# Kernel tuning notes

Hardware: AMD Instinct MI355X
Metric: run time of the kernel (lower is better)

Reference implementation:

```python
import jax, jax.numpy as jnp
import numpy as np

B, T, C = 32, 1024, 256   # T must equal block_size for the mask broadcast to be valid
HS = 64                   # head_size


def setup_inputs() -> dict:
    key = jax.random.key(0)
    kx, kk, kq, kv = jax.random.split(key, 4)
    s = 1.0 / np.sqrt(C)  # nn.Linear default-ish scale
    return {
        "x": jax.random.normal(kx, (B, T, C), dtype=jnp.float32),
        "Wk": jax.random.uniform(kk, (HS, C), dtype=jnp.float32, minval=-s, maxval=s),
        "Wq": jax.random.uniform(kq, (HS, C), dtype=jnp.float32, minval=-s, maxval=s),
        "Wv": jax.random.uniform(kv, (HS, C), dtype=jnp.float32, minval=-s, maxval=s),
    }


def reference(x, Wk, Wq, Wv):
    # projections: nn.Linear(bias=False) -> x @ W^T
    k = jnp.einsum('btc,hc->bth', x, Wk)  # [B,T,HS]
    q = jnp.einsum('btc,hc->bth', x, Wq)
    v = jnp.einsum('btc,hc->bth', x, Wv)
    # fresh cache + T == block_size  =>  k_cache = k, v_cache = v
    wei = jnp.einsum('bth,bsh->bts', q, k) / np.sqrt(HS)  # [B,T,T]
    causal = jnp.tril(jnp.ones((T, T), dtype=bool))
    wei = jnp.where(causal, wei, -jnp.inf)
    wei = jax.nn.softmax(wei, axis=-1)  # dropout p=0 -> identity
    out = jnp.einsum('bts,bsh->bth', wei, v)  # [B,T,HS]
    return out
```

## Files before the change

### kernel.cpp

```cpp
#include <hip/hip_runtime.h>
#include <hip/hip_bf16.h>
#include <math.h>


#define B_  32
#define T_  1024
#define C_  256
#define HS_ 64
#define QSCALE 0.1803368801111204f

typedef __attribute__((ext_vector_type(8))) short bf16x8;
typedef __attribute__((ext_vector_type(4))) float f32x4;

static __device__ __forceinline__ unsigned short f2bf(float f) {
    unsigned u = __builtin_bit_cast(unsigned, f);
    u += 0x7FFFu + ((u >> 16) & 1u);
    return (unsigned short)(u >> 16);
}
static __device__ __forceinline__ unsigned pack_bf2(float a, float b) {
    unsigned ua = __builtin_bit_cast(unsigned, a) + 0x8000u;
    unsigned ub = __builtin_bit_cast(unsigned, b) + 0x8000u;
    return __builtin_amdgcn_perm(ub, ua, 0x07060302u);
}
static __device__ __forceinline__ bf16x8 cvt8r(float4 v0, float4 v1) {
    union { bf16x8 v; unsigned u[4]; } t;
    t.u[0] = pack_bf2(v0.x, v0.y); t.u[1] = pack_bf2(v0.z, v0.w);
    t.u[2] = pack_bf2(v1.x, v1.y); t.u[3] = pack_bf2(v1.z, v1.w);
    return t.v;
}
static __device__ __forceinline__ float fexp2(float x) {
#if __has_builtin(__builtin_amdgcn_exp2f)
    return __builtin_amdgcn_exp2f(x);
#else
    return exp2f(x);
#endif
}
static __device__ __forceinline__ void gl_lds16(const float* g, void* l) {
    __builtin_amdgcn_global_load_lds(
        (const __attribute__((address_space(1))) unsigned*)g,
        (__attribute__((address_space(3))) unsigned*)l, 16, 0, 0);
}

__global__ __launch_bounds__(256) void prep_kernel(
    const float* __restrict__ Wk, const float* __restrict__ Wq,
    const float* __restrict__ Wv, unsigned short* __restrict__ wbf)
{
    const int idx = blockIdx.x * 256 + threadIdx.x;
    const int row = idx >> 6, c4 = (idx & 63) << 2;
    const float* src; float sc = 1.0f;
    if (row < 64)       src = &Wk[(size_t)row * C_];
    else if (row < 128) { src = &Wq[(size_t)(row - 64) * C_]; sc = QSCALE; }
    else                src = &Wv[(size_t)(row - 128) * C_];
    float4 v = *(const float4*)&src[c4];
    uint2 o = make_uint2(pack_bf2(v.x * sc, v.y * sc), pack_bf2(v.z * sc, v.w * sc));
    *(uint2*)&wbf[(size_t)row * C_ + c4] = o;
}

#define XPITCH 1040
__global__ __launch_bounds__(256) void proj_kernel(
    const float* __restrict__ x, const unsigned short* __restrict__ wbf,
    unsigned short* __restrict__ fqk, unsigned short* __restrict__ vt2)
{
    __shared__ __align__(16) char xls[32 * XPITCH];

    const int tid = threadIdx.x;
    const int lane = tid & 63, w = tid >> 6;
    const int q4 = lane >> 4, l15 = lane & 15;
    const int m0 = blockIdx.x * 32;

    {
        const float* gbase = &x[(size_t)(m0 + 8 * w) * C_ + lane * 4];
        #pragma unroll
        for (int j = 0; j < 8; ++j)
            gl_lds16(gbase + (size_t)j * C_, xls + (8 * w + j) * XPITCH);
    }

    const unsigned short* wrow = &wbf[(size_t)(48 * w + l15) * C_ + q4 * 8];

    f32x4 acc[3][2];
    #pragma unroll
    for (int nt = 0; nt < 3; ++nt)
        #pragma unroll
        for (int mt = 0; mt < 2; ++mt) acc[nt][mt] = (f32x4)0.0f;

    bf16x8 aw[3];
    #pragma unroll
    for (int nt = 0; nt < 3; ++nt)
        aw[nt] = *(const bf16x8*)&wrow[(size_t)nt * 16 * C_];

    __syncthreads();

    #pragma unroll
    for (int ks = 0; ks < 8; ++ks) {
        bf16x8 bx[2];
        #pragma unroll
        for (int mt = 0; mt < 2; ++mt) {
            const float* p = (const float*)(xls + (mt * 16 + l15) * XPITCH
                                            + (ks * 32 + q4 * 8) * 4);
            float4 v0 = *(const float4*)p;
            float4 v1 = *(const float4*)(p + 4);
            bx[mt] = cvt8r(v0, v1);
        }
        bf16x8 awn[3];
        if (ks < 7) {
            #pragma unroll
            for (int nt = 0; nt < 3; ++nt)
                awn[nt] = *(const bf16x8*)&wrow[(size_t)nt * 16 * C_ + (ks + 1) * 32];
        }
        #pragma unroll
        for (int nt = 0; nt < 3; ++nt) {
            acc[nt][0] = __builtin_amdgcn_mfma_f32_16x16x32_bf16(aw[nt], bx[0], acc[nt][0], 0, 0, 0);
            acc[nt][1] = __builtin_amdgcn_mfma_f32_16x16x32_bf16(aw[nt], bx[1], acc[nt][1], 0, 0, 0);
        }
        #pragma unroll
        for (int nt = 0; nt < 3; ++nt) aw[nt] = awn[nt];
    }

    const int mbg = m0 >> 4;
    #pragma unroll
    for (int nt = 0; nt < 3; ++nt) {
        const int c = 48 * w + 16 * nt + 4 * q4;
        #pragma unroll
        for (int mt = 0; mt < 2; ++mt) {
            const int m = m0 + mt * 16 + l15;
            f32x4 v = acc[nt][mt];
            if (c < 128) {
                uint2 o = make_uint2(pack_bf2(v.x, v.y), pack_bf2(v.z, v.w));
                *(uint2*)&fqk[(size_t)(mbg + mt) * 2048 + (c >> 3) * 128 + l15 * 8 + (c & 7)] = o;
            } else {
                const int batch = m >> 10, s = m & 1023;
                const int hb = c - 128;
                const int ht = hb >> 4, rb = hb & 15;
                const int sc = s >> 5, kk = s & 31;
                unsigned short* dst = &vt2[((((size_t)batch * 4 + ht) * 32 + sc) * 16) * 32
                                           + rb * 32 + kk];
                dst[0 * 32] = f2bf(v.x);
                dst[1 * 32] = f2bf(v.y);
                dst[2 * 32] = f2bf(v.z);
                dst[3 * 32] = f2bf(v.w);
            }
        }
    }
}

__global__ __launch_bounds__(256) void attn_kernel(
    const unsigned short* __restrict__ fqk,
    const unsigned short* __restrict__ vt2,
    float* __restrict__ out)
{
    __shared__ __align__(16) char smem[34816];

    const int tid = threadIdx.x;
    const int lane = tid & 63, w = tid >> 6;
    const int q4 = lane >> 4, l15 = lane & 15;
    const int slot  = blockIdx.x >> 3;
    const int batch = (blockIdx.x & 7) * 4 + (slot & 3);
    const int qt    = 31 - (slot >> 2);
    const int q0    = qt * 32;
    const int ns    = (qt >> 1) + 1;

    unsigned short (*Ps)[72] = (unsigned short(*)[72])(smem + w * 4608);

    const unsigned short* kb2 = &fqk[(size_t)batch * 64 * 2048];
    const unsigned short* vb2 = &vt2[(size_t)batch * 4 * 32 * 512];

    bf16x8 qf[2][2];
    #pragma unroll
    for (int it = 0; it < 2; ++it)
        #pragma unroll
        for (int kc = 0; kc < 2; ++kc)
            qf[it][kc] = *(const bf16x8*)&kb2[(size_t)((q0 >> 4) + it) * 2048
                                              + (8 + 4 * kc + q4) * 128 + l15 * 8];

    f32x4 o[4][2];
    #pragma unroll
    for (int ht = 0; ht < 4; ++ht)
        #pragma unroll
        for (int it = 0; it < 2; ++it) o[ht][it] = (f32x4)0.0f;
    float l[2] = {0.f, 0.f};

    for (int st = w; st < ns; st += 4) {
        const int s0 = st * 64;
        const bool last = (st == ns - 1);
        #pragma unroll
        for (int hf = 0; hf < 2; ++hf) {
            const int sh = s0 + hf * 32;
            bf16x8 ak[2][2];
            #pragma unroll
            for (int st16 = 0; st16 < 2; ++st16)
                #pragma unroll
                for (int kc = 0; kc < 2; ++kc)
                    ak[st16][kc] = *(const bf16x8*)&kb2[(size_t)((sh >> 4) + st16) * 2048
                                                        + (4 * kc + q4) * 128 + l15 * 8];
            bf16x8 av[4];
            #pragma unroll
            for (int ht = 0; ht < 4; ++ht)
                av[ht] = *(const bf16x8*)&vb2[((size_t)ht * 32 + (sh >> 5)) * 512
                                               + l15 * 32 + q4 * 8];
            f32x4 s[2][2];
            #pragma unroll
            for (int st16 = 0; st16 < 2; ++st16)
                #pragma unroll
                for (int it = 0; it < 2; ++it) {
                    f32x4 c = (f32x4)0.0f;
                    c = __builtin_amdgcn_mfma_f32_16x16x32_bf16(ak[st16][0], qf[it][0], c, 0, 0, 0);
                    c = __builtin_amdgcn_mfma_f32_16x16x32_bf16(ak[st16][1], qf[it][1], c, 0, 0, 0);
                    s[st16][it] = c;
                }
            #pragma unroll
            for (int st16 = 0; st16 < 2; ++st16)
                #pragma unroll
                for (int it = 0; it < 2; ++it) {
                    const int iloc = it * 16 + l15;
                    float p[4];
                    #pragma unroll
                    for (int r = 0; r < 4; ++r) {
                        float pv = fexp2(s[st16][it][r]);
                        if (last) {
                            int sl = sh + st16 * 16 + q4 * 4 + r;
                            if (sl > q0 + iloc) pv = 0.0f;
                        }
                        p[r] = pv;
                        l[it] += pv;
                    }
                    uint2 pw = make_uint2(pack_bf2(p[0], p[1]), pack_bf2(p[2], p[3]));
                    *(uint2*)&Ps[iloc][hf * 32 + st16 * 16 + q4 * 4] = pw;
                }
            #pragma unroll
            for (int it = 0; it < 2; ++it) {
                bf16x8 bp = *(const bf16x8*)&Ps[it * 16 + l15][hf * 32 + q4 * 8];
                #pragma unroll
                for (int ht = 0; ht < 4; ++ht)
                    o[ht][it] = __builtin_amdgcn_mfma_f32_16x16x32_bf16(av[ht], bp, o[ht][it], 0, 0, 0);
            }
        }
    }

    #pragma unroll
    for (int it = 0; it < 2; ++it) {
        l[it] += __shfl_xor(l[it], 16);
        l[it] += __shfl_xor(l[it], 32);
    }

    __syncthreads();
    float4* ocomb = (float4*)smem;
    float*  lcomb = (float*)(smem + 32768);
    #pragma unroll
    for (int ht = 0; ht < 4; ++ht)
        #pragma unroll
        for (int it = 0; it < 2; ++it) {
            f32x4 v = o[ht][it];
            ocomb[((w * 4 + ht) * 2 + it) * 64 + lane] = make_float4(v.x, v.y, v.z, v.w);
        }
    #pragma unroll
    for (int it = 0; it < 2; ++it) lcomb[(w * 2 + it) * 64 + lane] = l[it];
    __syncthreads();

    #pragma unroll
    for (int it = 0; it < 2; ++it) {
        float4 a = make_float4(0.f, 0.f, 0.f, 0.f);
        float lt = 0.f;
        #pragma unroll
        for (int src = 0; src < 4; ++src) {
            float4 t = ocomb[((src * 4 + w) * 2 + it) * 64 + lane];
            a.x += t.x; a.y += t.y; a.z += t.z; a.w += t.w;
            lt += lcomb[(src * 2 + it) * 64 + lane];
        }
        float inv = 1.0f / lt;
        float4 res = make_float4(a.x * inv, a.y * inv, a.z * inv, a.w * inv);
        *(float4*)&out[(size_t)(batch * T_ + q0 + it * 16 + l15) * HS_ + w * 16 + q4 * 4] = res;
    }
}

extern "C" void kernel_launch(void* const* d_in, const int* in_sizes, int n_in,
                              void* d_out, int out_size, void* d_ws, size_t ws_size,
                              hipStream_t stream) {
    (void)in_sizes; (void)n_in; (void)out_size; (void)ws_size;
    const float* x  = (const float*)d_in[0];
    const float* Wk = (const float*)d_in[1];
    const float* Wq = (const float*)d_in[2];
    const float* Wv = (const float*)d_in[3];

    unsigned short* wbf = (unsigned short*)d_ws;
    unsigned short* fqk = (unsigned short*)((char*)d_ws + 98304);
    unsigned short* vt2 = (unsigned short*)((char*)d_ws + 98304 + (size_t)32768 * 128 * 2);

    hipLaunchKernelGGL(prep_kernel, dim3(48),   dim3(256), 0, stream, Wk, Wq, Wv, wbf);
    hipLaunchKernelGGL(proj_kernel, dim3(1024), dim3(256), 0, stream, x, wbf, fqk, vt2);
    hipLaunchKernelGGL(attn_kernel, dim3(1024), dim3(256), 0, stream, fqk, vt2, (float*)d_out);
}
```

Before: 106.7 us.

## Fuse weight prep, projection and attention into one kernel with grid barrier

Merges the three launches into a single persistent-style kernel: weights are converted to bf16 (with the Q scale) inline during the projection GEMM, and an atomic-counter grid barrier separates the projection phase from the attention phase. This removes two kernel launches and the intermediate weight buffer. In exchange, every block must be co-resident for the spin barrier to be safe (1024 blocks at 4 per CU relies on enough CUs), a memset launch is added, and weights are reconverted from fp32 by every block.

```diff
diff --git a/kernel.cpp b/kernel.cpp
--- a/kernel.cpp
+++ b/kernel.cpp
@@ -8,6 +8,7 @@
 #define C_  256
 #define HS_ 64
 #define QSCALE 0.1803368801111204f
+#define NBLK 1024
 
 typedef __attribute__((ext_vector_type(8))) short bf16x8;
 typedef __attribute__((ext_vector_type(4))) float f32x4;
@@ -26,6 +27,12 @@
     union { bf16x8 v; unsigned u[4]; } t;
     t.u[0] = pack_bf2(v0.x, v0.y); t.u[1] = pack_bf2(v0.z, v0.w);
     t.u[2] = pack_bf2(v1.x, v1.y); t.u[3] = pack_bf2(v1.z, v1.w);
+    return t.v;
+}
+static __device__ __forceinline__ bf16x8 cvt8rs(float4 v0, float4 v1, float sc) {
+    union { bf16x8 v; unsigned u[4]; } t;
+    t.u[0] = pack_bf2(v0.x * sc, v0.y * sc); t.u[1] = pack_bf2(v0.z * sc, v0.w * sc);
+    t.u[2] = pack_bf2(v1.x * sc, v1.y * sc); t.u[3] = pack_bf2(v1.z * sc, v1.w * sc);
     return t.v;
 }
 static __device__ __forceinline__ float fexp2(float x) {
@@ -41,234 +48,242 @@
         (__attribute__((address_space(3))) unsigned*)l, 16, 0, 0);
 }
 
-__global__ __launch_bounds__(256) void prep_kernel(
+#define XPITCH 1040
+
+__global__ __launch_bounds__(256, 4) void fused_kernel(
+    const float* __restrict__ x,
     const float* __restrict__ Wk, const float* __restrict__ Wq,
-    const float* __restrict__ Wv, unsigned short* __restrict__ wbf)
+    const float* __restrict__ Wv,
+    unsigned short* __restrict__ fqk, unsigned short* __restrict__ vt2,
+    unsigned* __restrict__ cnt, float* __restrict__ out)
 {
-    const int idx = blockIdx.x * 256 + threadIdx.x;
-    const int row = idx >> 6, c4 = (idx & 63) << 2;
-    const float* src; float sc = 1.0f;
-    if (row < 64)       src = &Wk[(size_t)row * C_];
-    else if (row < 128) { src = &Wq[(size_t)(row - 64) * C_]; sc = QSCALE; }
-    else                src = &Wv[(size_t)(row - 128) * C_];
-    float4 v = *(const float4*)&src[c4];
-    uint2 o = make_uint2(pack_bf2(v.x * sc, v.y * sc), pack_bf2(v.z * sc, v.w * sc));
-    *(uint2*)&wbf[(size_t)row * C_ + c4] = o;
-}
-
-#define XPITCH 1040
-__global__ __launch_bounds__(256) void proj_kernel(
-    const float* __restrict__ x, const unsigned short* __restrict__ wbf,
-    unsigned short* __restrict__ fqk, unsigned short* __restrict__ vt2)
-{
-    __shared__ __align__(16) char xls[32 * XPITCH];
+    __shared__ __align__(16) char smem[34816];
 
     const int tid = threadIdx.x;
     const int lane = tid & 63, w = tid >> 6;
     const int q4 = lane >> 4, l15 = lane & 15;
-    const int m0 = blockIdx.x * 32;
 
     {
-        const float* gbase = &x[(size_t)(m0 + 8 * w) * C_ + lane * 4];
-        #pragma unroll
-        for (int j = 0; j < 8; ++j)
-            gl_lds16(gbase + (size_t)j * C_, xls + (8 * w + j) * XPITCH);
+        char* xls = smem;
+        const int m0 = blockIdx.x * 32;
+
+        {
+            const float* gbase = &x[(size_t)(m0 + 8 * w) * C_ + lane * 4];
+            #pragma unroll
+            for (int j = 0; j < 8; ++j)
+                gl_lds16(gbase + (size_t)j * C_, xls + (8 * w + j) * XPITCH);
+        }
+
+        const float* wp[3];
+        float wsc[3];
+        #pragma unroll
+        for (int nt = 0; nt < 3; ++nt) {
+            const int nb = 48 * w + nt * 16;
+            if (nb < 64)       { wp[nt] = &Wk[(size_t)(nb       + l15) * C_ + q4 * 8]; wsc[nt] = 1.0f; }
+            else if (nb < 128) { wp[nt] = &Wq[(size_t)(nb - 64  + l15) * C_ + q4 * 8]; wsc[nt] = QSCALE; }
+            else               { wp[nt] = &Wv[(size_t)(nb - 128 + l15) * C_ + q4 * 8]; wsc[nt] = 1.0f; }
+        }
+
+        f32x4 acc[3][2];
+        #pragma unroll
+        for (int nt = 0; nt < 3; ++nt)
+            #pragma unroll
+            for (int mt = 0; mt < 2; ++mt) acc[nt][mt] = (f32x4)0.0f;
+
+        float4 aw[6];
+        #pragma unroll
+        for (int nt = 0; nt < 3; ++nt) {
+            aw[2 * nt]     = *(const float4*)(wp[nt]);
+            aw[2 * nt + 1] = *(const float4*)(wp[nt] + 4);
+        }
+
+        __syncthreads();
+
+        #pragma unroll
+        for (int ks = 0; ks < 8; ++ks) {
+            bf16x8 bx[2];
+            #pragma unroll
+            for (int mt = 0; mt < 2; ++mt) {
+                const float* p = (const float*)(xls + (mt * 16 + l15) * XPITCH
+                                                + (ks * 32 + q4 * 8) * 4);
+                float4 v0 = *(const float4*)p;
+                float4 v1 = *(const float4*)(p + 4);
+                bx[mt] = cvt8r(v0, v1);
+            }
+            float4 awn[6];
+            if (ks < 7) {
+                #pragma unroll
+                for (int nt = 0; nt < 3; ++nt) {
+                    awn[2 * nt]     = *(const float4*)(wp[nt] + (ks + 1) * 32);
+                    awn[2 * nt + 1] = *(const float4*)(wp[nt] + (ks + 1) * 32 + 4);
+                }
+            }
+            #pragma unroll
+            for (int nt = 0; nt < 3; ++nt) {
+                bf16x8 a = cvt8rs(aw[2 * nt], aw[2 * nt + 1], wsc[nt]);
+                acc[nt][0] = __builtin_amdgcn_mfma_f32_16x16x32_bf16(a, bx[0], acc[nt][0], 0, 0, 0);
+                acc[nt][1] = __builtin_amdgcn_mfma_f32_16x16x32_bf16(a, bx[1], acc[nt][1], 0, 0, 0);
+            }
+            #pragma unroll
+            for (int j = 0; j < 6; ++j) aw[j] = awn[j];
+        }
+
+        const int mbg = m0 >> 4;
+        #pragma unroll
+        for (int nt = 0; nt < 3; ++nt) {
+            const int c = 48 * w + 16 * nt + 4 * q4;
+            #pragma unroll
+            for (int mt = 0; mt < 2; ++mt) {
+                const int m = m0 + mt * 16 + l15;
+                f32x4 v = acc[nt][mt];
+                if (c < 128) {
+                    uint2 o = make_uint2(pack_bf2(v.x, v.y), pack_bf2(v.z, v.w));
+                    *(uint2*)&fqk[(size_t)(mbg + mt) * 2048 + (c >> 3) * 128 + l15 * 8 + (c & 7)] = o;
+                } else {
+                    const int batch = m >> 10, s = m & 1023;
+                    const int hb = c - 128;
+                    const int ht = hb >> 4, rb = hb & 15;
+                    const int sc = s >> 5, kk = s & 31;
+                    unsigned short* dst = &vt2[((((size_t)batch * 4 + ht) * 32 + sc) * 16) * 32
+                                               + rb * 32 + kk];
+                    dst[0 * 32] = f2bf(v.x);
+                    dst[1 * 32] = f2bf(v.y);
+                    dst[2 * 32] = f2bf(v.z);
+                    dst[3 * 32] = f2bf(v.w);
+                }
+            }
+        }
     }
 
-    const unsigned short* wrow = &wbf[(size_t)(48 * w + l15) * C_ + q4 * 8];
-
-    f32x4 acc[3][2];
-    #pragma unroll
-    for (int nt = 0; nt < 3; ++nt)
-        #pragma unroll
-        for (int mt = 0; mt < 2; ++mt) acc[nt][mt] = (f32x4)0.0f;
-
-    bf16x8 aw[3];
-    #pragma unroll
-    for (int nt = 0; nt < 3; ++nt)
-        aw[nt] = *(const bf16x8*)&wrow[(size_t)nt * 16 * C_];
-
     __syncthreads();
-
-    #pragma unroll
-    for (int ks = 0; ks < 8; ++ks) {
-        bf16x8 bx[2];
-        #pragma unroll
-        for (int mt = 0; mt < 2; ++mt) {
-            const float* p = (const float*)(xls + (mt * 16 + l15) * XPITCH
-                                            + (ks * 32 + q4 * 8) * 4);
-            float4 v0 = *(const float4*)p;
-            float4 v1 = *(const float4*)(p + 4);
-            bx[mt] = cvt8r(v0, v1);
-        }
-        bf16x8 awn[3];
-        if (ks < 7) {
-            #pragma unroll
-            for (int nt = 0; nt < 3; ++nt)
-                awn[nt] = *(const bf16x8*)&wrow[(size_t)nt * 16 * C_ + (ks + 1) * 32];
-        }
-        #pragma unroll
-        for (int nt = 0; nt < 3; ++nt) {
-            acc[nt][0] = __builtin_amdgcn_mfma_f32_16x16x32_bf16(aw[nt], bx[0], acc[nt][0], 0, 0, 0);
-            acc[nt][1] = __builtin_amdgcn_mfma_f32_16x16x32_bf16(aw[nt], bx[1], acc[nt][1], 0, 0, 0);
-        }
-        #pragma unroll
-        for (int nt = 0; nt < 3; ++nt) aw[nt] = awn[nt];
+    if (tid == 0) {
+        __threadfence();
+        atomicAdd(cnt, 1u);
+        while (__hip_atomic_load(cnt, __ATOMIC_RELAXED, __HIP_MEMORY_SCOPE_AGENT)
+               < (unsigned)NBLK)
+            __builtin_amdgcn_s_sleep(2);
+        __threadfence();
     }
-
-    const int mbg = m0 >> 4;
-    #pragma unroll
-    for (int nt = 0; nt < 3; ++nt) {
-        const int c = 48 * w + 16 * nt + 4 * q4;
-        #pragma unroll
-        for (int mt = 0; mt < 2; ++mt) {
-            const int m = m0 + mt * 16 + l15;
-            f32x4 v = acc[nt][mt];
-            if (c < 128) {
-                uint2 o = make_uint2(pack_bf2(v.x, v.y), pack_bf2(v.z, v.w));
-                *(uint2*)&fqk[(size_t)(mbg + mt) * 2048 + (c >> 3) * 128 + l15 * 8 + (c & 7)] = o;
-            } else {
-                const int batch = m >> 10, s = m & 1023;
-                const int hb = c - 128;
-                const int ht = hb >> 4, rb = hb & 15;
-                const int sc = s >> 5, kk = s & 31;
-                unsigned short* dst = &vt2[((((size_t)batch * 4 + ht) * 32 + sc) * 16) * 32
-                                           + rb * 32 + kk];
-                dst[0 * 32] = f2bf(v.x);
-                dst[1 * 32] = f2bf(v.y);
-                dst[2 * 32] = f2bf(v.z);
-                dst[3 * 32] = f2bf(v.w);
-            }
-        }
-    }
-}
-
-__global__ __launch_bounds__(256) void attn_kernel(
-    const unsigned short* __restrict__ fqk,
-    const unsigned short* __restrict__ vt2,
-    float* __restrict__ out)
-{
-    __shared__ __align__(16) char smem[34816];
-
-    const int tid = threadIdx.x;
-    const int lane = tid & 63, w = tid >> 6;
-    const int q4 = lane >> 4, l15 = lane & 15;
-    const int slot  = blockIdx.x >> 3;
-    const int batch = (blockIdx.x & 7) * 4 + (slot & 3);
-    const int qt    = 31 - (slot >> 2);
-    const int q0    = qt * 32;
-    const int ns    = (qt >> 1) + 1;
-
-    unsigned short (*Ps)[72] = (unsigned short(*)[72])(smem + w * 4608);
-
-    const unsigned short* kb2 = &fqk[(size_t)batch * 64 * 2048];
-    const unsigned short* vb2 = &vt2[(size_t)batch * 4 * 32 * 512];
-
-    bf16x8 qf[2][2];
-    #pragma unroll
-    for (int it = 0; it < 2; ++it)
-        #pragma unroll
-        for (int kc = 0; kc < 2; ++kc)
-            qf[it][kc] = *(const bf16x8*)&kb2[(size_t)((q0 >> 4) + it) * 2048
-                                              + (8 + 4 * kc + q4) * 128 + l15 * 8];
-
-    f32x4 o[4][2];
-    #pragma unroll
-    for (int ht = 0; ht < 4; ++ht)
-        #pragma unroll
-        for (int it = 0; it < 2; ++it) o[ht][it] = (f32x4)0.0f;
-    float l[2] = {0.f, 0.f};
-
-    for (int st = w; st < ns; st += 4) {
-        const int s0 = st * 64;
-        const bool last = (st == ns - 1);
-        #pragma unroll
-        for (int hf = 0; hf < 2; ++hf) {
-            const int sh = s0 + hf * 32;
-            bf16x8 ak[2][2];
-            #pragma unroll
-            for (int st16 = 0; st16 < 2; ++st16)
-                #pragma unroll
-                for (int kc = 0; kc < 2; ++kc)
-                    ak[st16][kc] = *(const bf16x8*)&kb2[(size_t)((sh >> 4) + st16) * 2048
-                                                        + (4 * kc + q4) * 128 + l15 * 8];
-            bf16x8 av[4];
-            #pragma unroll
-            for (int ht = 0; ht < 4; ++ht)
-                av[ht] = *(const bf16x8*)&vb2[((size_t)ht * 32 + (sh >> 5)) * 512
-                                               + l15 * 32 + q4 * 8];
-            f32x4 s[2][2];
-            #pragma unroll
-            for (int st16 = 0; st16 < 2; ++st16)
+    __syncthreads();
+
+    {
+        const int slot  = blockIdx.x >> 3;
+        const int batch = (blockIdx.x & 7) * 4 + (slot & 3);
+        const int qt    = 31 - (slot >> 2);
+        const int q0    = qt * 32;
+        const int ns    = (qt >> 1) + 1;
+
+        unsigned short (*Ps)[72] = (unsigned short(*)[72])(smem + w * 4608);
+
+        const unsigned short* kb2 = &fqk[(size_t)batch * 64 * 2048];
+        const unsigned short* vb2 = &vt2[(size_t)batch * 4 * 32 * 512];
+
+        bf16x8 qf[2][2];
+        #pragma unroll
+        for (int it = 0; it < 2; ++it)
+            #pragma unroll
+            for (int kc = 0; kc < 2; ++kc)
+                qf[it][kc] = *(const bf16x8*)&kb2[(size_t)((q0 >> 4) + it) * 2048
+                                                  + (8 + 4 * kc + q4) * 128 + l15 * 8];
+
+        f32x4 o[4][2];
+        #pragma unroll
+        for (int ht = 0; ht < 4; ++ht)
+            #pragma unroll
+            for (int it = 0; it < 2; ++it) o[ht][it] = (f32x4)0.0f;
+        float l[2] = {0.f, 0.f};
+
+        for (int st = w; st < ns; st += 4) {
+            const int s0 = st * 64;
+            const bool last = (st == ns - 1);
+            #pragma unroll
+            for (int hf = 0; hf < 2; ++hf) {
+                const int sh = s0 + hf * 32;
+                bf16x8 ak[2][2];
+                #pragma unroll
+                for (int st16 = 0; st16 < 2; ++st16)
+                    #pragma unroll
+                    for (int kc = 0; kc < 2; ++kc)
+                        ak[st16][kc] = *(const bf16x8*)&kb2[(size_t)((sh >> 4) + st16) * 2048
+                                                            + (4 * kc + q4) * 128 + l15 * 8];
+                bf16x8 av[4];
+                #pragma unroll
+                for (int ht = 0; ht < 4; ++ht)
+                    av[ht] = *(const bf16x8*)&vb2[((size_t)ht * 32 + (sh >> 5)) * 512
+                                                   + l15 * 32 + q4 * 8];
+                f32x4 s[2][2];
+                #pragma unroll
+                for (int st16 = 0; st16 < 2; ++st16)
+                    #pragma unroll
+                    for (int it = 0; it < 2; ++it) {
+                        f32x4 c = (f32x4)0.0f;
+                        c = __builtin_amdgcn_mfma_f32_16x16x32_bf16(ak[st16][0], qf[it][0], c, 0, 0, 0);
+                        c = __builtin_amdgcn_mfma_f32_16x16x32_bf16(ak[st16][1], qf[it][1], c, 0, 0, 0);
+                        s[st16][it] = c;
+                    }
+                #pragma unroll
+                for (int st16 = 0; st16 < 2; ++st16)
+                    #pragma unroll
+                    for (int it = 0; it < 2; ++it) {
+                        const int iloc = it * 16 + l15;
+                        float p[4];
+                        #pragma unroll
+                        for (int r = 0; r < 4; ++r) {
+                            float pv = fexp2(s[st16][it][r]);
+                            if (last) {
+                                int sl = sh + st16 * 16 + q4 * 4 + r;
+                                if (sl > q0 + iloc) pv = 0.0f;
+                            }
+                            p[r] = pv;
+                            l[it] += pv;
+                        }
+                        uint2 pw = make_uint2(pack_bf2(p[0], p[1]), pack_bf2(p[2], p[3]));
+                        *(uint2*)&Ps[iloc][hf * 32 + st16 * 16 + q4 * 4] = pw;
+                    }
                 #pragma unroll
                 for (int it = 0; it < 2; ++it) {
-                    f32x4 c = (f32x4)0.0f;
-                    c = __builtin_amdgcn_mfma_f32_16x16x32_bf16(ak[st16][0], qf[it][0], c, 0, 0, 0);
-                    c = __builtin_amdgcn_mfma_f32_16x16x32_bf16(ak[st16][1], qf[it][1], c, 0, 0, 0);
-                    s[st16][it] = c;
+                    bf16x8 bp = *(const bf16x8*)&Ps[it * 16 + l15][hf * 32 + q4 * 8];
+                    #pragma unroll
+                    for (int ht = 0; ht < 4; ++ht)
+                        o[ht][it] = __builtin_amdgcn_mfma_f32_16x16x32_bf16(av[ht], bp, o[ht][it], 0, 0, 0);
                 }
-            #pragma unroll
-            for (int st16 = 0; st16 < 2; ++st16)
-                #pragma unroll
-                for (int it = 0; it < 2; ++it) {
-                    const int iloc = it * 16 + l15;
-                    float p[4];
-                    #pragma unroll
-                    for (int r = 0; r < 4; ++r) {
-                        float pv = fexp2(s[st16][it][r]);
-                        if (last) {
-                            int sl = sh + st16 * 16 + q4 * 4 + r;
-                            if (sl > q0 + iloc) pv = 0.0f;
-                        }
-                        p[r] = pv;
-                        l[it] += pv;
-                    }
-                    uint2 pw = make_uint2(pack_bf2(p[0], p[1]), pack_bf2(p[2], p[3]));
-                    *(uint2*)&Ps[iloc][hf * 32 + st16 * 16 + q4 * 4] = pw;
-                }
+            }
+        }
+
+        #pragma unroll
+        for (int it = 0; it < 2; ++it) {
+            l[it] += __shfl_xor(l[it], 16);
+            l[it] += __shfl_xor(l[it], 32);
+        }
+
+        __syncthreads();
+        float4* ocomb = (float4*)smem;
+        float*  lcomb = (float*)(smem + 32768);
+        #pragma unroll
+        for (int ht = 0; ht < 4; ++ht)
             #pragma unroll
             for (int it = 0; it < 2; ++it) {
-                bf16x8 bp = *(const bf16x8*)&Ps[it * 16 + l15][hf * 32 + q4 * 8];
-                #pragma unroll
-                for (int ht = 0; ht < 4; ++ht)
-                    o[ht][it] = __builtin_amdgcn_mfma_f32_16x16x32_bf16(av[ht], bp, o[ht][it], 0, 0, 0);
-            }
-        }
-    }
-
-    #pragma unroll
-    for (int it = 0; it < 2; ++it) {
-        l[it] += __shfl_xor(l[it], 16);
-        l[it] += __shfl_xor(l[it], 32);
-    }
-
-    __syncthreads();
-    float4* ocomb = (float4*)smem;
-    float*  lcomb = (float*)(smem + 32768);
-    #pragma unroll
-    for (int ht = 0; ht < 4; ++ht)
+                f32x4 v = o[ht][it];
+                ocomb[((w * 4 + ht) * 2 + it) * 64 + lane] = make_float4(v.x, v.y, v.z, v.w);
+            }
+        #pragma unroll
+        for (int it = 0; it < 2; ++it) lcomb[(w * 2 + it) * 64 + lane] = l[it];
+        __syncthreads();
+
         #pragma unroll
         for (int it = 0; it < 2; ++it) {
-            f32x4 v = o[ht][it];
-            ocomb[((w * 4 + ht) * 2 + it) * 64 + lane] = make_float4(v.x, v.y, v.z, v.w);
-        }
-    #pragma unroll
-    for (int it = 0; it < 2; ++it) lcomb[(w * 2 + it) * 64 + lane] = l[it];
-    __syncthreads();
-
-    #pragma unroll
-    for (int it = 0; it < 2; ++it) {
-        float4 a = make_float4(0.f, 0.f, 0.f, 0.f);
-        float lt = 0.f;
-        #pragma unroll
-        for (int src = 0; src < 4; ++src) {
-            float4 t = ocomb[((src * 4 + w) * 2 + it) * 64 + lane];
-            a.x += t.x; a.y += t.y; a.z += t.z; a.w += t.w;
-            lt += lcomb[(src * 2 + it) * 64 + lane];
-        }
-        float inv = 1.0f / lt;
-        float4 res = make_float4(a.x * inv, a.y * inv, a.z * inv, a.w * inv);
-        *(float4*)&out[(size_t)(batch * T_ + q0 + it * 16 + l15) * HS_ + w * 16 + q4 * 4] = res;
+            float4 a = make_float4(0.f, 0.f, 0.f, 0.f);
+            float lt = 0.f;
+            #pragma unroll
+            for (int src = 0; src < 4; ++src) {
+                float4 t = ocomb[((src * 4 + w) * 2 + it) * 64 + lane];
+                a.x += t.x; a.y += t.y; a.z += t.z; a.w += t.w;
+                lt += lcomb[(src * 2 + it) * 64 + lane];
+            }
+            float inv = 1.0f / lt;
+            float4 res = make_float4(a.x * inv, a.y * inv, a.z * inv, a.w * inv);
+            *(float4*)&out[(size_t)(batch * T_ + q0 + it * 16 + l15) * HS_ + w * 16 + q4 * 4] = res;
+        }
     }
 }
 
@@ -281,11 +296,11 @@
     const float* Wq = (const float*)d_in[2];
     const float* Wv = (const float*)d_in[3];
 
-    unsigned short* wbf = (unsigned short*)d_ws;
-    unsigned short* fqk = (unsigned short*)((char*)d_ws + 98304);
-    unsigned short* vt2 = (unsigned short*)((char*)d_ws + 98304 + (size_t)32768 * 128 * 2);
-
-    hipLaunchKernelGGL(prep_kernel, dim3(48),   dim3(256), 0, stream, Wk, Wq, Wv, wbf);
-    hipLaunchKernelGGL(proj_kernel, dim3(1024), dim3(256), 0, stream, x, wbf, fqk, vt2);
-    hipLaunchKernelGGL(attn_kernel, dim3(1024), dim3(256), 0, stream, fqk, vt2, (float*)d_out);
-}
+    unsigned short* fqk = (unsigned short*)d_ws;
+    unsigned short* vt2 = (unsigned short*)((char*)d_ws + (size_t)32768 * 128 * 2);
+    unsigned* cnt = (unsigned*)((char*)d_ws + (16u << 20));
+
+    hipMemsetAsync(cnt, 0, 128, stream);
+    hipLaunchKernelGGL(fused_kernel, dim3(NBLK), dim3(256), 0, stream,
+                       x, Wk, Wq, Wv, fqk, vt2, cnt, (float*)d_out);
+}
```

Result: slower. 244.6 us (+129.2%).
